# Performance work log

Hardware: AMD Instinct MI355X
Metric: run time of the kernel (lower is better)

The kernel has to match this reference:

```python
import jax, jax.numpy as jnp
import numpy as np

B, N, D, FF = 4096, 8, 256, 2048
EPS = 1e-5


def _layernorm(x, gamma, beta):
    mu = jnp.mean(x, axis=-1, keepdims=True)
    var = jnp.mean((x - mu) ** 2, axis=-1, keepdims=True)
    return (x - mu) * jax.lax.rsqrt(var + EPS) * gamma + beta


def _tt_product(x, w):
    # x: [b, d_in, n], w: [d_in, d_out, n]
    # h[:, :, k] = sum_i x[:, :, i] @ w[:, :, (k - i) % n]  (circular contraction)
    n = x.shape[-1]
    k = jnp.arange(n)
    idx = (k[:, None] - k[None, :]) % n          # [k, i]
    wg = w[:, :, idx]                            # [d_in, d_out, k, i]
    return jnp.einsum('bdi,doki->bok', x, wg)    # [b, d_out, n]


def setup_inputs() -> dict:
    key = jax.random.key(0)
    ks = jax.random.split(key, 12)
    xav = lambda k, shp, fi, fo: jax.random.uniform(k, shp, jnp.float32, -1.0, 1.0) * np.sqrt(6.0 / (fi + fo))
    return {
        'ent_seq': jax.random.normal(ks[0], (B, N, D), jnp.float32),
        'w_in': xav(ks[1], (D, D, N), D, D),
        'w_out': xav(ks[2], (D, D, N), D, D),
        'W1': xav(ks[3], (FF, D), D, FF),
        'bias1': jnp.zeros((FF,), jnp.float32),
        'W2': xav(ks[4], (D, FF), FF, D),
        'bias2': jnp.zeros((D,), jnp.float32),
        'gamma1': jnp.ones((D,), jnp.float32),
        'beta1': jnp.zeros((D,), jnp.float32),
        'gamma2': jnp.ones((D,), jnp.float32),
        'beta2': jnp.zeros((D,), jnp.float32),
    }


def reference(ent_seq, w_in, w_out, W1, bias1, W2, bias2, gamma1, beta1, gamma2, beta2):
    # self-attention-like block (dropout = identity in eval mode)
    xn = _layernorm(ent_seq, gamma1, beta1)          # [B, N, D]
    xp = jnp.transpose(xn, (0, 2, 1))                # [B, D, N]
    half = xp.shape[0] // 2
    h = jnp.concatenate([_tt_product(xp[:half], w_in),
                         _tt_product(xp[half:], w_out)], axis=0)
    x = ent_seq + jnp.transpose(h, (0, 2, 1))        # residual
    # FFN block
    yn = _layernorm(x, gamma2, beta2)
    ff = jax.nn.relu(yn @ W1.T + bias1) @ W2.T + bias2
    return x + ff
```

## Files before the change

### kernel.cpp

```cpp
#include <hip/hip_runtime.h>
#include <hip/hip_bf16.h>

typedef unsigned short ushort_t;
typedef __attribute__((ext_vector_type(8))) short bf16x8;
typedef __attribute__((ext_vector_type(4))) float f32x4;

#define B_SZ 4096
#define N_SZ 8
#define D_SZ 256
#define FF_SZ 2048
#define M_SZ (B_SZ * N_SZ)
#define WELEM (D_SZ * D_SZ * N_SZ)

__device__ inline float b2f(ushort_t u) {
    union { unsigned int i; float f; } t; t.i = ((unsigned int)u) << 16; return t.f;
}
__device__ inline ushort_t f2b(float f) {
    union { unsigned int i; float f; } t; t.f = f;
    unsigned int i = t.i;
    unsigned int r = (i + 0x7fffu + ((i >> 16) & 1u)) >> 16;
    return (ushort_t)r;
}

__device__ inline void gl2lds16(const ushort_t* g, ushort_t* l) {
    __builtin_amdgcn_global_load_lds((const __attribute__((address_space(1))) void*)g,
                                     (__attribute__((address_space(3))) void*)l, 16, 0, 0);
}

__global__ __launch_bounds__(256) void convert_weights(const float* __restrict__ w_in,
                                                       const float* __restrict__ w_out,
                                                       const float* __restrict__ W1,
                                                       const float* __restrict__ W2,
                                                       ushort_t* __restrict__ bt_in,
                                                       ushort_t* __restrict__ bt_out,
                                                       ushort_t* __restrict__ W1b,
                                                       ushort_t* __restrict__ W2b) {
    __shared__ float tile[64][65];
    const int bid = blockIdx.x;
    const int t = threadIdx.x;
    if (bid < 256) {
        const float* w = (bid < 128) ? w_in : w_out;
        ushort_t* bt = (bid < 128) ? bt_in : bt_out;
        const int id = bid & 127;
        const int d10 = (id >> 5) * 64;
        const int j0  = (id & 31) * 64;
#pragma unroll
        for (int it = 0; it < 16; ++it) {
            const int d1l = it * 4 + (t >> 6);
            const int jl = t & 63;
            tile[d1l][jl] = w[(size_t)(d10 + d1l) * 2048 + j0 + jl];
        }
        __syncthreads();
#pragma unroll
        for (int it = 0; it < 16; ++it) {
            const int jl = it * 4 + (t >> 6);
            const int d1l = t & 63;
            const int j = j0 + jl;
            bt[(size_t)(j >> 3) * 2048 + (j & 7) * 256 + d10 + d1l] = f2b(tile[d1l][jl]);
        }
    } else {
        const int id = bid - 256;
        const float* w = (id < 256) ? W1 : W2;
        ushort_t* o = (id < 256) ? W1b : W2b;
        const size_t base = (size_t)(id & 255) * 2048 + t * 8;
        const float4 a = *(const float4*)&w[base];
        const float4 b = *(const float4*)&w[base + 4];
        *(ushort4*)&o[base]     = make_ushort4(f2b(a.x), f2b(a.y), f2b(a.z), f2b(a.w));
        *(ushort4*)&o[base + 4] = make_ushort4(f2b(b.x), f2b(b.y), f2b(b.z), f2b(b.w));
    }
}

__global__ __launch_bounds__(256) void ln_fast(const float* __restrict__ xin,
                                               const float* __restrict__ gam,
                                               const float* __restrict__ bet,
                                               ushort_t* __restrict__ out) {
    const int wave = threadIdx.x >> 6;
    const int lane = threadIdx.x & 63;
    const size_t row = (size_t)blockIdx.x * 4 + wave;
    const float4 v = *(const float4*)&xin[row * 256 + lane * 4];
    float s = v.x + v.y + v.z + v.w;
    float q = v.x * v.x + v.y * v.y + v.z * v.z + v.w * v.w;
#pragma unroll
    for (int off = 1; off < 64; off <<= 1) {
        s += __shfl_xor(s, off, 64);
        q += __shfl_xor(q, off, 64);
    }
    const float mu = s * (1.0f / 256.0f);
    const float var = q * (1.0f / 256.0f) - mu * mu;
    const float rs = rsqrtf(var + 1e-5f);
    const float4 g = *(const float4*)&gam[lane * 4];
    const float4 b = *(const float4*)&bet[lane * 4];
    ushort4 o;
    o.x = f2b((v.x - mu) * rs * g.x + b.x);
    o.y = f2b((v.y - mu) * rs * g.y + b.y);
    o.z = f2b((v.z - mu) * rs * g.z + b.z);
    o.w = f2b((v.w - mu) * rs * g.w + b.w);
    *(ushort4*)&out[row * 256 + lane * 4] = o;
}

#define HSTR 264

__global__ __launch_bounds__(256, 2) void tt_ln2(const ushort_t* __restrict__ A,
                                                 const ushort_t* __restrict__ Bt0,
                                                 const ushort_t* __restrict__ Bt1,
                                                 const float* __restrict__ g2,
                                                 const float* __restrict__ be2,
                                                 const float* __restrict__ entf,
                                                 ushort_t* __restrict__ yn,
                                                 ushort_t* __restrict__ xb) {
    __shared__ __attribute__((aligned(16))) ushort_t As[64 * 64];
    __shared__ __attribute__((aligned(16))) ushort_t Bs[256 * 64];
    __shared__ float red_s[64 * 4];
    __shared__ float red_q[64 * 4];

    const int t = threadIdx.x;
    const int lb = ((blockIdx.x & 1) << 8) | (blockIdx.x >> 1);
    const int m0 = lb * 64;
    const int lane = t & 63;
    const int wc = t >> 6;
    const int l16 = lane & 15, quad = lane >> 4;
    const int tr = t >> 3;
    const int csw = (((t & 7) ^ (tr & 7)) << 3);

    const ushort_t* Bt = (m0 >= M_SZ / 2) ? Bt1 : Bt0;

    f32x4 acc[4][4];
#pragma unroll
    for (int i = 0; i < 4; i++)
#pragma unroll
        for (int j = 0; j < 4; j++) acc[i][j] = (f32x4)(0.0f);

#pragma unroll 1
    for (int kt = 0; kt < 32; ++kt) {
        const int kg = kt * 64;
        __syncthreads();
#pragma unroll
        for (int p = 0; p < 2; ++p) {
            const int mrow = m0 + p * 32 + tr;
            const int kcol = kg + csw;
            const int s = kcol >> 8;
            const ushort_t* gA = A + (size_t)((mrow & ~7) + (((mrow & 7) - s) & 7)) * 256 + (kcol & 255);
            gl2lds16(gA, As + p * 2048 + t * 8);
        }
#pragma unroll
        for (int p = 0; p < 8; ++p) {
            gl2lds16(Bt + (size_t)(p * 32 + tr) * 2048 + kg + csw, Bs + p * 2048 + t * 8);
        }
        __syncthreads();

#pragma unroll
        for (int kk = 0; kk < 2; ++kk) {
            const int ac = ((((kk << 2) | quad) ^ (l16 & 7)) << 3);
            bf16x8 af[4], bfv[4];
#pragma unroll
            for (int i = 0; i < 4; i++) af[i]  = *(const bf16x8*)&As[(i * 16 + l16) * 64 + ac];
#pragma unroll
            for (int j = 0; j < 4; j++) bfv[j] = *(const bf16x8*)&Bs[(wc * 64 + j * 16 + l16) * 64 + ac];
#pragma unroll
            for (int i = 0; i < 4; i++)
#pragma unroll
                for (int j = 0; j < 4; j++)
                    acc[i][j] = __builtin_amdgcn_mfma_f32_16x16x32_bf16(af[i], bfv[j], acc[i][j], 0, 0, 0);
        }
    }

    int c[4];
#pragma unroll
    for (int j = 0; j < 4; j++) c[j] = wc * 64 + j * 16 + l16;
#pragma unroll
    for (int i = 0; i < 4; i++) {
#pragma unroll
        for (int r = 0; r < 4; r++) {
            const int rl = i * 16 + quad * 4 + r;
            const size_t grow = (size_t)(m0 + rl) * 256;
            float s = 0.0f, q = 0.0f;
#pragma unroll
            for (int j = 0; j < 4; j++) {
                float v = acc[i][j][r] + entf[grow + c[j]];
                acc[i][j][r] = v;
                s += v;
                q += v * v;
            }
#pragma unroll
            for (int off = 1; off < 16; off <<= 1) {
                s += __shfl_xor(s, off, 64);
                q += __shfl_xor(q, off, 64);
            }
            if (l16 == 0) { red_s[rl * 4 + wc] = s; red_q[rl * 4 + wc] = q; }
        }
    }
    __syncthreads();
#pragma unroll
    for (int i = 0; i < 4; i++) {
#pragma unroll
        for (int r = 0; r < 4; r++) {
            const int rl = i * 16 + quad * 4 + r;
            const size_t grow = (size_t)(m0 + rl) * 256;
            const float4 ss = *(const float4*)&red_s[rl * 4];
            const float4 qq = *(const float4*)&red_q[rl * 4];
            const float S = ss.x + ss.y + ss.z + ss.w;
            const float Q = qq.x + qq.y + qq.z + qq.w;
            const float mu = S * (1.0f / 256.0f);
            const float var = Q * (1.0f / 256.0f) - mu * mu;
            const float rs = rsqrtf(var + 1e-5f);
#pragma unroll
            for (int j = 0; j < 4; j++) {
                const float v = acc[i][j][r];
                yn[grow + c[j]] = f2b((v - mu) * rs * g2[c[j]] + be2[c[j]]);
                xb[grow + c[j]] = f2b(v);
            }
        }
    }
}

__global__ __launch_bounds__(256, 2) void ff_fused(const ushort_t* __restrict__ yn,
                                                   const ushort_t* __restrict__ W1b,
                                                   const ushort_t* __restrict__ W2b,
                                                   const float* __restrict__ bias1,
                                                   const float* __restrict__ bias2,
                                                   const ushort_t* __restrict__ xb,
                                                   float* __restrict__ out) {
    __shared__ __attribute__((aligned(16))) ushort_t As[64 * 64];
    __shared__ __attribute__((aligned(16))) ushort_t Bs[256 * 64];
    __shared__ __attribute__((aligned(16))) ushort_t Hc[64 * HSTR];

    const int t = threadIdx.x;
    const int m0 = blockIdx.x * 64;
    const int lane = t & 63;
    const int wc = t >> 6;
    const int l16 = lane & 15, quad = lane >> 4;
    const int tr = t >> 3;
    const int csw = (((t & 7) ^ (tr & 7)) << 3);

    f32x4 acc2[4][4];
#pragma unroll
    for (int i = 0; i < 4; i++)
#pragma unroll
        for (int j = 0; j < 4; j++) acc2[i][j] = (f32x4)(0.0f);

    int c4[4];
#pragma unroll
    for (int j = 0; j < 4; j++) c4[j] = wc * 64 + j * 16 + l16;

#pragma unroll 1
    for (int c = 0; c < 8; ++c) {
        f32x4 acc1[4][4];
#pragma unroll
        for (int i = 0; i < 4; i++)
#pragma unroll
            for (int j = 0; j < 4; j++) acc1[i][j] = (f32x4)(0.0f);

#pragma unroll 1
        for (int kb = 0; kb < 4; ++kb) {
            const int kg = kb * 64;
            __syncthreads();
#pragma unroll
            for (int p = 0; p < 2; ++p)
                gl2lds16(yn + (size_t)(m0 + p * 32 + tr) * 256 + kg + csw, As + p * 2048 + t * 8);
#pragma unroll
            for (int p = 0; p < 8; ++p)
                gl2lds16(W1b + (size_t)(c * 256 + p * 32 + tr) * 256 + kg + csw, Bs + p * 2048 + t * 8);
            __syncthreads();
#pragma unroll
            for (int kk = 0; kk < 2; ++kk) {
                const int ac = ((((kk << 2) | quad) ^ (l16 & 7)) << 3);
                bf16x8 af[4], bfv[4];
#pragma unroll
                for (int i = 0; i < 4; i++) af[i]  = *(const bf16x8*)&As[(i * 16 + l16) * 64 + ac];
#pragma unroll
                for (int j = 0; j < 4; j++) bfv[j] = *(const bf16x8*)&Bs[(wc * 64 + j * 16 + l16) * 64 + ac];
#pragma unroll
                for (int i = 0; i < 4; i++)
#pragma unroll
                    for (int j = 0; j < 4; j++)
                        acc1[i][j] = __builtin_amdgcn_mfma_f32_16x16x32_bf16(af[i], bfv[j], acc1[i][j], 0, 0, 0);
            }
        }

#pragma unroll
        for (int j = 0; j < 4; j++) {
            const float bb = bias1[c * 256 + c4[j]];
#pragma unroll
            for (int i = 0; i < 4; i++) {
                const int rbase = i * 16 + quad * 4;
#pragma unroll
                for (int r = 0; r < 4; r++) {
                    float v = acc1[i][j][r] + bb;
                    v = v > 0.0f ? v : 0.0f;
                    Hc[(rbase + r) * HSTR + c4[j]] = f2b(v);
                }
            }
        }

#pragma unroll 1
        for (int kb = 0; kb < 4; ++kb) {
            __syncthreads();
#pragma unroll
            for (int p = 0; p < 8; ++p)
                gl2lds16(W2b + (size_t)(p * 32 + tr) * 2048 + c * 256 + kb * 64 + csw, Bs + p * 2048 + t * 8);
            __syncthreads();
#pragma unroll
            for (int kk = 0; kk < 2; ++kk) {
                const int ank = kb * 64 + (((kk << 2) | quad) << 3);
                const int ac  = ((((kk << 2) | quad) ^ (l16 & 7)) << 3);
                bf16x8 af[4], bfv[4];
#pragma unroll
                for (int i = 0; i < 4; i++) af[i]  = *(const bf16x8*)&Hc[(i * 16 + l16) * HSTR + ank];
#pragma unroll
                for (int j = 0; j < 4; j++) bfv[j] = *(const bf16x8*)&Bs[(wc * 64 + j * 16 + l16) * 64 + ac];
#pragma unroll
                for (int i = 0; i < 4; i++)
#pragma unroll
                    for (int j = 0; j < 4; j++)
                        acc2[i][j] = __builtin_amdgcn_mfma_f32_16x16x32_bf16(af[i], bfv[j], acc2[i][j], 0, 0, 0);
            }
        }
    }

#pragma unroll
    for (int j = 0; j < 4; j++) {
        const float b2 = bias2[c4[j]];
#pragma unroll
        for (int i = 0; i < 4; i++) {
            const int rbase = m0 + i * 16 + quad * 4;
#pragma unroll
            for (int r = 0; r < 4; r++) {
                const size_t o = (size_t)(rbase + r) * 256 + c4[j];
                out[o] = acc2[i][j][r] + b2 + b2f(xb[o]);
            }
        }
    }
}

extern "C" void kernel_launch(void* const* d_in, const int* in_sizes, int n_in,
                              void* d_out, int out_size, void* d_ws, size_t ws_size,
                              hipStream_t stream) {
    const float* ent   = (const float*)d_in[0];
    const float* w_in  = (const float*)d_in[1];
    const float* w_out = (const float*)d_in[2];
    const float* W1    = (const float*)d_in[3];
    const float* bias1 = (const float*)d_in[4];
    const float* W2    = (const float*)d_in[5];
    const float* bias2 = (const float*)d_in[6];
    const float* g1    = (const float*)d_in[7];
    const float* be1   = (const float*)d_in[8];
    const float* g2    = (const float*)d_in[9];
    const float* be2   = (const float*)d_in[10];
    float* out = (float*)d_out;

    char* ws = (char*)d_ws;
    ushort_t* xn     = (ushort_t*)ws;
    ushort_t* yn     = (ushort_t*)(ws + 16777216);
    ushort_t* xb     = (ushort_t*)(ws + 2 * 16777216);
    ushort_t* bt_in  = (ushort_t*)(ws + 3 * 16777216);
    ushort_t* bt_out = bt_in + WELEM;
    ushort_t* W1b    = bt_out + WELEM;
    ushort_t* W2b    = W1b + WELEM;

    convert_weights<<<dim3(768), dim3(256), 0, stream>>>(w_in, w_out, W1, W2,
                                                         bt_in, bt_out, W1b, W2b);
    ln_fast<<<dim3(M_SZ / 4), dim3(256), 0, stream>>>(ent, g1, be1, xn);
    tt_ln2<<<dim3(M_SZ / 64), dim3(256), 0, stream>>>(xn, bt_in, bt_out, g2, be2, ent, yn, xb);
    ff_fused<<<dim3(M_SZ / 64), dim3(256), 0, stream>>>(yn, W1b, W2b, bias1, bias2, xb, out);
}
```

Measured before the change: 241.9 us.

## Split TT GEMM into larger-tile split-K kernel plus separate residual-LayerNorm combine

Replaces the fused TT-product+LayerNorm kernel with a 256x256-tile, 512-thread GEMM that splits K in two and double-buffers LDS stages, writing fp32 partial sums. A new combine kernel adds the two partials and the residual, then computes LayerNorm2 and writes bf16 outputs. This aims to cut repeated weight reloads and overlap loads with MFMA, at the cost of 64MB of extra fp32 partial traffic and an additional launch.

```diff
diff --git a/kernel.cpp b/kernel.cpp
--- a/kernel.cpp
+++ b/kernel.cpp
@@ -98,121 +98,127 @@
     *(ushort4*)&out[row * 256 + lane * 4] = o;
 }
 
-#define HSTR 264
-
-__global__ __launch_bounds__(256, 2) void tt_ln2(const ushort_t* __restrict__ A,
-                                                 const ushort_t* __restrict__ Bt0,
-                                                 const ushort_t* __restrict__ Bt1,
-                                                 const float* __restrict__ g2,
-                                                 const float* __restrict__ be2,
-                                                 const float* __restrict__ entf,
-                                                 ushort_t* __restrict__ yn,
-                                                 ushort_t* __restrict__ xb) {
-    __shared__ __attribute__((aligned(16))) ushort_t As[64 * 64];
-    __shared__ __attribute__((aligned(16))) ushort_t Bs[256 * 64];
-    __shared__ float red_s[64 * 4];
-    __shared__ float red_q[64 * 4];
+
+__global__ __launch_bounds__(512, 2) void tt_ks64(const ushort_t* __restrict__ A,
+                                                  const ushort_t* __restrict__ Bt0,
+                                                  const ushort_t* __restrict__ Bt1,
+                                                  float* __restrict__ P) {
+    __shared__ __attribute__((aligned(16))) ushort_t As[2][256 * 64];
+    __shared__ __attribute__((aligned(16))) ushort_t Bs[2][256 * 64];
 
     const int t = threadIdx.x;
-    const int lb = ((blockIdx.x & 1) << 8) | (blockIdx.x >> 1);
-    const int m0 = lb * 64;
+    const int mtile = blockIdx.x & 127;
+    const int kh = blockIdx.x >> 7;
+    const int m0 = mtile * 256;
+    const int k0 = kh * 1024;
     const int lane = t & 63;
-    const int wc = t >> 6;
+    const int wave = t >> 6;
+    const int wr = wave >> 2, wc = wave & 3;
     const int l16 = lane & 15, quad = lane >> 4;
     const int tr = t >> 3;
     const int csw = (((t & 7) ^ (tr & 7)) << 3);
 
     const ushort_t* Bt = (m0 >= M_SZ / 2) ? Bt1 : Bt0;
-
-    f32x4 acc[4][4];
-#pragma unroll
-    for (int i = 0; i < 4; i++)
+    float* Pk = P + (size_t)kh * M_SZ * 256;
+
+    f32x4 acc[8][4];
+#pragma unroll
+    for (int i = 0; i < 8; i++)
 #pragma unroll
         for (int j = 0; j < 4; j++) acc[i][j] = (f32x4)(0.0f);
 
-#pragma unroll 1
-    for (int kt = 0; kt < 32; ++kt) {
-        const int kg = kt * 64;
-        __syncthreads();
-#pragma unroll
-        for (int p = 0; p < 2; ++p) {
-            const int mrow = m0 + p * 32 + tr;
+    auto stage = [&](int kt) {
+        ushort_t* a = As[kt & 1];
+        ushort_t* b = Bs[kt & 1];
+        const int kg = k0 + kt * 64;
+#pragma unroll
+        for (int p = 0; p < 4; ++p) {
+            const int mrow = m0 + p * 64 + tr;
             const int kcol = kg + csw;
             const int s = kcol >> 8;
             const ushort_t* gA = A + (size_t)((mrow & ~7) + (((mrow & 7) - s) & 7)) * 256 + (kcol & 255);
-            gl2lds16(gA, As + p * 2048 + t * 8);
-        }
-#pragma unroll
-        for (int p = 0; p < 8; ++p) {
-            gl2lds16(Bt + (size_t)(p * 32 + tr) * 2048 + kg + csw, Bs + p * 2048 + t * 8);
-        }
+            gl2lds16(gA, a + p * 4096 + t * 8);
+        }
+#pragma unroll
+        for (int p = 0; p < 4; ++p) {
+            gl2lds16(Bt + (size_t)(p * 64 + tr) * 2048 + kg + csw, b + p * 4096 + t * 8);
+        }
+    };
+
+    stage(0);
+#pragma unroll 1
+    for (int kt = 0; kt < 16; ++kt) {
         __syncthreads();
-
+        if (kt < 15) stage(kt + 1);
+        const ushort_t* a = As[kt & 1];
+        const ushort_t* b = Bs[kt & 1];
 #pragma unroll
         for (int kk = 0; kk < 2; ++kk) {
             const int ac = ((((kk << 2) | quad) ^ (l16 & 7)) << 3);
-            bf16x8 af[4], bfv[4];
-#pragma unroll
-            for (int i = 0; i < 4; i++) af[i]  = *(const bf16x8*)&As[(i * 16 + l16) * 64 + ac];
-#pragma unroll
-            for (int j = 0; j < 4; j++) bfv[j] = *(const bf16x8*)&Bs[(wc * 64 + j * 16 + l16) * 64 + ac];
-#pragma unroll
-            for (int i = 0; i < 4; i++)
+            bf16x8 af[8], bfv[4];
+#pragma unroll
+            for (int i = 0; i < 8; i++) af[i]  = *(const bf16x8*)&a[(wr * 128 + i * 16 + l16) * 64 + ac];
+#pragma unroll
+            for (int j = 0; j < 4; j++) bfv[j] = *(const bf16x8*)&b[(wc * 64 + j * 16 + l16) * 64 + ac];
+#pragma unroll
+            for (int i = 0; i < 8; i++)
 #pragma unroll
                 for (int j = 0; j < 4; j++)
                     acc[i][j] = __builtin_amdgcn_mfma_f32_16x16x32_bf16(af[i], bfv[j], acc[i][j], 0, 0, 0);
         }
     }
 
-    int c[4];
-#pragma unroll
-    for (int j = 0; j < 4; j++) c[j] = wc * 64 + j * 16 + l16;
-#pragma unroll
-    for (int i = 0; i < 4; i++) {
-#pragma unroll
-        for (int r = 0; r < 4; r++) {
-            const int rl = i * 16 + quad * 4 + r;
-            const size_t grow = (size_t)(m0 + rl) * 256;
-            float s = 0.0f, q = 0.0f;
-#pragma unroll
-            for (int j = 0; j < 4; j++) {
-                float v = acc[i][j][r] + entf[grow + c[j]];
-                acc[i][j][r] = v;
-                s += v;
-                q += v * v;
-            }
-#pragma unroll
-            for (int off = 1; off < 16; off <<= 1) {
-                s += __shfl_xor(s, off, 64);
-                q += __shfl_xor(q, off, 64);
-            }
-            if (l16 == 0) { red_s[rl * 4 + wc] = s; red_q[rl * 4 + wc] = q; }
-        }
-    }
-    __syncthreads();
-#pragma unroll
-    for (int i = 0; i < 4; i++) {
-#pragma unroll
-        for (int r = 0; r < 4; r++) {
-            const int rl = i * 16 + quad * 4 + r;
-            const size_t grow = (size_t)(m0 + rl) * 256;
-            const float4 ss = *(const float4*)&red_s[rl * 4];
-            const float4 qq = *(const float4*)&red_q[rl * 4];
-            const float S = ss.x + ss.y + ss.z + ss.w;
-            const float Q = qq.x + qq.y + qq.z + qq.w;
-            const float mu = S * (1.0f / 256.0f);
-            const float var = Q * (1.0f / 256.0f) - mu * mu;
-            const float rs = rsqrtf(var + 1e-5f);
-#pragma unroll
-            for (int j = 0; j < 4; j++) {
-                const float v = acc[i][j][r];
-                yn[grow + c[j]] = f2b((v - mu) * rs * g2[c[j]] + be2[c[j]]);
-                xb[grow + c[j]] = f2b(v);
-            }
-        }
-    }
-}
-
+#pragma unroll
+    for (int j = 0; j < 4; j++) {
+        const int coln = wc * 64 + j * 16 + l16;
+#pragma unroll
+        for (int i = 0; i < 8; i++) {
+            const int rbase = m0 + wr * 128 + i * 16 + quad * 4;
+#pragma unroll
+            for (int rr = 0; rr < 4; rr++)
+                Pk[(size_t)(rbase + rr) * 256 + coln] = acc[i][j][rr];
+        }
+    }
+}
+
+__global__ __launch_bounds__(256) void tt_combine(const float* __restrict__ P,
+                                                  const float* __restrict__ ent,
+                                                  const float* __restrict__ g2,
+                                                  const float* __restrict__ be2,
+                                                  ushort_t* __restrict__ yn,
+                                                  ushort_t* __restrict__ xb) {
+    const int wave = threadIdx.x >> 6;
+    const int lane = threadIdx.x & 63;
+    const size_t row = (size_t)blockIdx.x * 4 + wave;
+    const size_t o = row * 256 + lane * 4;
+    const float4 a = *(const float4*)&P[o];
+    const float4 b = *(const float4*)&P[(size_t)M_SZ * 256 + o];
+    const float4 e = *(const float4*)&ent[o];
+    float4 v;
+    v.x = a.x + b.x + e.x; v.y = a.y + b.y + e.y;
+    v.z = a.z + b.z + e.z; v.w = a.w + b.w + e.w;
+    float s = v.x + v.y + v.z + v.w;
+    float q = v.x * v.x + v.y * v.y + v.z * v.z + v.w * v.w;
+#pragma unroll
+    for (int off = 1; off < 64; off <<= 1) {
+        s += __shfl_xor(s, off, 64);
+        q += __shfl_xor(q, off, 64);
+    }
+    const float mu = s * (1.0f / 256.0f);
+    const float var = q * (1.0f / 256.0f) - mu * mu;
+    const float rs = rsqrtf(var + 1e-5f);
+    const float4 g = *(const float4*)&g2[lane * 4];
+    const float4 be = *(const float4*)&be2[lane * 4];
+    ushort4 yo, xo;
+    yo.x = f2b((v.x - mu) * rs * g.x + be.x); xo.x = f2b(v.x);
+    yo.y = f2b((v.y - mu) * rs * g.y + be.y); xo.y = f2b(v.y);
+    yo.z = f2b((v.z - mu) * rs * g.z + be.z); xo.z = f2b(v.z);
+    yo.w = f2b((v.w - mu) * rs * g.w + be.w); xo.w = f2b(v.w);
+    *(ushort4*)&yn[o] = yo;
+    *(ushort4*)&xb[o] = xo;
+}
+
+#define HSTR 264
 __global__ __launch_bounds__(256, 2) void ff_fused(const ushort_t* __restrict__ yn,
                                                    const ushort_t* __restrict__ W1b,
                                                    const ushort_t* __restrict__ W2b,
@@ -356,10 +362,12 @@
     ushort_t* bt_out = bt_in + WELEM;
     ushort_t* W1b    = bt_out + WELEM;
     ushort_t* W2b    = W1b + WELEM;
+    float*    P      = (float*)(ws + 54525952);
 
     convert_weights<<<dim3(768), dim3(256), 0, stream>>>(w_in, w_out, W1, W2,
                                                          bt_in, bt_out, W1b, W2b);
     ln_fast<<<dim3(M_SZ / 4), dim3(256), 0, stream>>>(ent, g1, be1, xn);
-    tt_ln2<<<dim3(M_SZ / 64), dim3(256), 0, stream>>>(xn, bt_in, bt_out, g2, be2, ent, yn, xb);
+    tt_ks64<<<dim3(256), dim3(512), 0, stream>>>(xn, bt_in, bt_out, P);
+    tt_combine<<<dim3(M_SZ / 4), dim3(256), 0, stream>>>(P, ent, g2, be2, yn, xb);
     ff_fused<<<dim3(M_SZ / 64), dim3(256), 0, stream>>>(yn, W1b, W2b, bias1, bias2, xb, out);
 }
```

Measured after the change: 254.1 us. +5.1%, slower.

## Enlarge TT GEMM tile to 256 rows with double-buffered LDS staging

Applied to the files above, without the earlier changes.

The circular tensor-train GEMM + LayerNorm kernel now uses 512-thread blocks covering 256 rows each (8 waves in a 2x4 grid) instead of 64 rows, so every loaded B tile is reused across four times as many rows. A and B tiles are double-buffered in LDS so the next K-slice is loaded while the current one is consumed, and one barrier per iteration is dropped. The cost is a grid of only 128 blocks and roughly 136KB of LDS per block, which limits residency to one block per CU. That risks leaving many CUs idle.

```diff
diff --git a/kernel.cpp b/kernel.cpp
--- a/kernel.cpp
+++ b/kernel.cpp
@@ -98,85 +98,92 @@
     *(ushort4*)&out[row * 256 + lane * 4] = o;
 }
 
-#define HSTR 264
-
-__global__ __launch_bounds__(256, 2) void tt_ln2(const ushort_t* __restrict__ A,
-                                                 const ushort_t* __restrict__ Bt0,
-                                                 const ushort_t* __restrict__ Bt1,
-                                                 const float* __restrict__ g2,
-                                                 const float* __restrict__ be2,
-                                                 const float* __restrict__ entf,
-                                                 ushort_t* __restrict__ yn,
-                                                 ushort_t* __restrict__ xb) {
-    __shared__ __attribute__((aligned(16))) ushort_t As[64 * 64];
-    __shared__ __attribute__((aligned(16))) ushort_t Bs[256 * 64];
-    __shared__ float red_s[64 * 4];
-    __shared__ float red_q[64 * 4];
+
+__global__ __launch_bounds__(512, 2) void tt_ln2_v2(const ushort_t* __restrict__ A,
+                                                    const ushort_t* __restrict__ Bt0,
+                                                    const ushort_t* __restrict__ Bt1,
+                                                    const float* __restrict__ g2,
+                                                    const float* __restrict__ be2,
+                                                    const float* __restrict__ entf,
+                                                    ushort_t* __restrict__ yn,
+                                                    ushort_t* __restrict__ xb) {
+    __shared__ __attribute__((aligned(16))) ushort_t As[2][256 * 64];
+    __shared__ __attribute__((aligned(16))) ushort_t Bs[2][256 * 64];
+    __shared__ float red_s[256 * 4];
+    __shared__ float red_q[256 * 4];
 
     const int t = threadIdx.x;
-    const int lb = ((blockIdx.x & 1) << 8) | (blockIdx.x >> 1);
-    const int m0 = lb * 64;
+    const int lb = ((blockIdx.x & 1) << 6) | (blockIdx.x >> 1);
+    const int m0 = lb * 256;
     const int lane = t & 63;
-    const int wc = t >> 6;
+    const int wave = t >> 6;
+    const int wr = wave >> 2, wc = wave & 3;
     const int l16 = lane & 15, quad = lane >> 4;
     const int tr = t >> 3;
     const int csw = (((t & 7) ^ (tr & 7)) << 3);
 
     const ushort_t* Bt = (m0 >= M_SZ / 2) ? Bt1 : Bt0;
 
-    f32x4 acc[4][4];
-#pragma unroll
-    for (int i = 0; i < 4; i++)
+    f32x4 acc[8][4];
+#pragma unroll
+    for (int i = 0; i < 8; i++)
 #pragma unroll
         for (int j = 0; j < 4; j++) acc[i][j] = (f32x4)(0.0f);
 
-#pragma unroll 1
-    for (int kt = 0; kt < 32; ++kt) {
+    auto stage = [&](int kt) {
+        ushort_t* a = As[kt & 1];
+        ushort_t* b = Bs[kt & 1];
         const int kg = kt * 64;
-        __syncthreads();
-#pragma unroll
-        for (int p = 0; p < 2; ++p) {
-            const int mrow = m0 + p * 32 + tr;
+#pragma unroll
+        for (int p = 0; p < 4; ++p) {
+            const int mrow = m0 + p * 64 + tr;
             const int kcol = kg + csw;
             const int s = kcol >> 8;
             const ushort_t* gA = A + (size_t)((mrow & ~7) + (((mrow & 7) - s) & 7)) * 256 + (kcol & 255);
-            gl2lds16(gA, As + p * 2048 + t * 8);
-        }
-#pragma unroll
-        for (int p = 0; p < 8; ++p) {
-            gl2lds16(Bt + (size_t)(p * 32 + tr) * 2048 + kg + csw, Bs + p * 2048 + t * 8);
-        }
+            gl2lds16(gA, a + p * 4096 + t * 8);
+        }
+#pragma unroll
+        for (int p = 0; p < 4; ++p) {
+            gl2lds16(Bt + (size_t)(p * 64 + tr) * 2048 + kg + csw, b + p * 4096 + t * 8);
+        }
+    };
+
+    stage(0);
+#pragma unroll 1
+    for (int kt = 0; kt < 32; ++kt) {
         __syncthreads();
-
+        if (kt < 31) stage(kt + 1);
+        const ushort_t* a = As[kt & 1];
+        const ushort_t* b = Bs[kt & 1];
 #pragma unroll
         for (int kk = 0; kk < 2; ++kk) {
             const int ac = ((((kk << 2) | quad) ^ (l16 & 7)) << 3);
-            bf16x8 af[4], bfv[4];
-#pragma unroll
-            for (int i = 0; i < 4; i++) af[i]  = *(const bf16x8*)&As[(i * 16 + l16) * 64 + ac];
-#pragma unroll
-            for (int j = 0; j < 4; j++) bfv[j] = *(const bf16x8*)&Bs[(wc * 64 + j * 16 + l16) * 64 + ac];
-#pragma unroll
-            for (int i = 0; i < 4; i++)
+            bf16x8 af[8], bfv[4];
+#pragma unroll
+            for (int i = 0; i < 8; i++) af[i]  = *(const bf16x8*)&a[(wr * 128 + i * 16 + l16) * 64 + ac];
+#pragma unroll
+            for (int j = 0; j < 4; j++) bfv[j] = *(const bf16x8*)&b[(wc * 64 + j * 16 + l16) * 64 + ac];
+#pragma unroll
+            for (int i = 0; i < 8; i++)
 #pragma unroll
                 for (int j = 0; j < 4; j++)
                     acc[i][j] = __builtin_amdgcn_mfma_f32_16x16x32_bf16(af[i], bfv[j], acc[i][j], 0, 0, 0);
         }
     }
 
-    int c[4];
-#pragma unroll
-    for (int j = 0; j < 4; j++) c[j] = wc * 64 + j * 16 + l16;
-#pragma unroll
-    for (int i = 0; i < 4; i++) {
+    int c4[4];
+#pragma unroll
+    for (int j = 0; j < 4; j++) c4[j] = wc * 64 + j * 16 + l16;
+#pragma unroll
+    for (int i = 0; i < 8; i++) {
 #pragma unroll
         for (int r = 0; r < 4; r++) {
-            const int rl = i * 16 + quad * 4 + r;
+            const int rl = wr * 128 + i * 16 + quad * 4 + r;
             const size_t grow = (size_t)(m0 + rl) * 256;
             float s = 0.0f, q = 0.0f;
 #pragma unroll
             for (int j = 0; j < 4; j++) {
-                float v = acc[i][j][r] + entf[grow + c[j]];
+                float v = acc[i][j][r] + entf[grow + c4[j]];
                 acc[i][j][r] = v;
                 s += v;
                 q += v * v;
@@ -191,10 +198,10 @@
     }
     __syncthreads();
 #pragma unroll
-    for (int i = 0; i < 4; i++) {
+    for (int i = 0; i < 8; i++) {
 #pragma unroll
         for (int r = 0; r < 4; r++) {
-            const int rl = i * 16 + quad * 4 + r;
+            const int rl = wr * 128 + i * 16 + quad * 4 + r;
             const size_t grow = (size_t)(m0 + rl) * 256;
             const float4 ss = *(const float4*)&red_s[rl * 4];
             const float4 qq = *(const float4*)&red_q[rl * 4];
@@ -206,13 +213,14 @@
 #pragma unroll
             for (int j = 0; j < 4; j++) {
                 const float v = acc[i][j][r];
-                yn[grow + c[j]] = f2b((v - mu) * rs * g2[c[j]] + be2[c[j]]);
-                xb[grow + c[j]] = f2b(v);
-            }
-        }
-    }
-}
-
+                yn[grow + c4[j]] = f2b((v - mu) * rs * g2[c4[j]] + be2[c4[j]]);
+                xb[grow + c4[j]] = f2b(v);
+            }
+        }
+    }
+}
+
+#define HSTR 264
 __global__ __launch_bounds__(256, 2) void ff_fused(const ushort_t* __restrict__ yn,
                                                    const ushort_t* __restrict__ W1b,
                                                    const ushort_t* __restrict__ W2b,
@@ -360,6 +368,6 @@
     convert_weights<<<dim3(768), dim3(256), 0, stream>>>(w_in, w_out, W1, W2,
                                                          bt_in, bt_out, W1b, W2b);
     ln_fast<<<dim3(M_SZ / 4), dim3(256), 0, stream>>>(ent, g1, be1, xn);
-    tt_ln2<<<dim3(M_SZ / 64), dim3(256), 0, stream>>>(xn, bt_in, bt_out, g2, be2, ent, yn, xb);
+    tt_ln2_v2<<<dim3(M_SZ / 256), dim3(512), 0, stream>>>(xn, bt_in, bt_out, g2, be2, ent, yn, xb);
     ff_fused<<<dim3(M_SZ / 64), dim3(256), 0, stream>>>(yn, W1b, W2b, bias1, bias2, xb, out);
 }
```

New measurement: 274.7 us. 1.14x slower.
